# Performance work log

Hardware: AMD Instinct MI355X
Metric: run time of the kernel (lower is better)

## Reference

```python
import jax, jax.numpy as jnp
import numpy as np
import math

EPS = 1e-6
C = 0.01

def _norm(x):
    return jnp.maximum(jnp.linalg.norm(x, axis=-1, keepdims=True), EPS)

def project_to_ball(x, c=C):
    max_norm = 1.0 / math.sqrt(c) - EPS
    norm = _norm(x)
    clamped = jnp.minimum(norm, max_norm - EPS)
    return x * (clamped / norm)

def log_map_zero(x, c=C):
    sqrt_c = math.sqrt(c)
    xn = _norm(x)
    scaled = jnp.minimum(sqrt_c * xn, 1.0 - EPS)
    return jnp.arctanh(scaled) * x / (sqrt_c * xn)

def exp_map_zero(v, c=C):
    sqrt_c = math.sqrt(c)
    vn = _norm(v)
    res = jnp.tanh(sqrt_c * vn) * (v / vn) / sqrt_c
    return project_to_ball(res, c)

def setup_inputs() -> dict:
    key = jax.random.key(0)
    k1, k2, k3 = jax.random.split(key, 3)
    N, d_in, d_out = 262144, 256, 256
    x = jax.random.normal(k1, (N, d_in), dtype=jnp.float32)
    # xavier_uniform with relu gain = sqrt(2)
    gain = math.sqrt(2.0)
    bound = gain * math.sqrt(6.0 / (d_in + d_out))
    W = jax.random.uniform(k2, (d_out, d_in), dtype=jnp.float32, minval=-bound, maxval=bound)
    b = jnp.zeros((d_out,), dtype=jnp.float32)
    return {"x": x, "W": W, "b": b}

def reference(x, W, b):
    tangent = log_map_zero(x)                      # [N, d_in]
    transformed = tangent @ W.T + b                # [N, d_out]
    return exp_map_zero(transformed)               # [N, d_out]
```

## Files before the change

### kernel.cpp

```cpp
#include <hip/hip_runtime.h>
#include <stdint.h>

typedef float f32x4 __attribute__((ext_vector_type(4)));
typedef __bf16 bf16x8 __attribute__((ext_vector_type(8)));

__device__ __forceinline__ unsigned int pack_bf16_rne(float fa, float fb) {
  unsigned int ua = __float_as_uint(fa);
  ua += 0x7fffu + ((ua >> 16) & 1u);
  unsigned int ub = __float_as_uint(fb);
  ub += 0x7fffu + ((ub >> 16) & 1u);
  return __builtin_amdgcn_perm(ub, ua, 0x07060302u);
}

__device__ __forceinline__ void async_cp16(const void* g, void* l) {
  __builtin_amdgcn_global_load_lds(
      (const __attribute__((address_space(1))) unsigned int*)g,
      (__attribute__((address_space(3))) unsigned int*)l, 16, 0, 0);
}

__global__ void wcvt_kernel(const float* __restrict__ W, uint2* __restrict__ Wb) {
  int i = blockIdx.x * blockDim.x + threadIdx.x;
  float4 v = ((const float4*)W)[i];
  uint2 o;
  o.x = pack_bf16_rne(v.x, v.y);
  o.y = pack_bf16_rne(v.z, v.w);
  Wb[i] = o;
}

__global__ __launch_bounds__(256) void hyper_kernel(
    const float* __restrict__ x, const unsigned short* __restrict__ Wb,
    const float* __restrict__ bias, float* __restrict__ out) {
  __shared__ __align__(16) unsigned char As[64 * 256 * 2];
  __shared__ __align__(16) unsigned char Bs[256 * 64 * 2];
  __shared__ float a_scale[64];
  __shared__ float rowsq[64][4];
  __shared__ float oscale[64];

  const int tid = threadIdx.x;
  const int row0 = blockIdx.x * 64;

  {
    const int r = tid >> 2;
    const int j = tid & 3;
    const float4* xr = (const float4*)(x + (size_t)(row0 + r) * 256);
    float ssq = 0.f;
#pragma unroll
    for (int i = 0; i < 8; ++i) {
      int q = j + 4 * i;
      float4 v0 = xr[q * 2];
      float4 v1 = xr[q * 2 + 1];
      ssq += v0.x * v0.x + v0.y * v0.y + v0.z * v0.z + v0.w * v0.w +
             v1.x * v1.x + v1.y * v1.y + v1.z * v1.z + v1.w * v1.w;
      uint4 pk;
      pk.x = pack_bf16_rne(v0.x, v0.y);
      pk.y = pack_bf16_rne(v0.z, v0.w);
      pk.z = pack_bf16_rne(v1.x, v1.y);
      pk.w = pack_bf16_rne(v1.z, v1.w);
      *(uint4*)(As + r * 512 + ((q ^ (r & 7)) << 4)) = pk;
    }
    ssq += __shfl_xor(ssq, 1);
    ssq += __shfl_xor(ssq, 2);
    if (j == 0) {
      float xn = fmaxf(sqrtf(ssq), 1e-6f);
      float t = fminf(0.1f * xn, 1.f - 1e-6f);
      a_scale[r] = atanhf(t) / (0.1f * xn);
    }
  }

  const int wv = tid >> 6;
  const int lane = tid & 63;
  const int l15 = lane & 15;
  const int l4 = lane >> 4;

  const f32x4 fzero = {0.f, 0.f, 0.f, 0.f};
  f32x4 acc[4][4];
#pragma unroll
  for (int a = 0; a < 4; ++a)
#pragma unroll
    for (int b = 0; b < 4; ++b) acc[a][b] = fzero;

  for (int kb = 0; kb < 4; ++kb) {
#pragma unroll
    for (int it = 0; it < 8; ++it) {
      int s = it * 256 + tid;
      int rr = s >> 3, cc = s & 7;
      const unsigned short* g = Wb + rr * 256 + kb * 64 + ((cc ^ (rr & 7)) << 3);
      async_cp16(g, Bs + s * 16);
    }
    __syncthreads();

#pragma unroll
    for (int kk = 0; kk < 2; ++kk) {
      bf16x8 af[4], bfr[4];
#pragma unroll
      for (int t = 0; t < 4; ++t) {
        int ar = t * 16 + l15;
        int qf = kb * 8 + kk * 4 + l4;
        af[t] = *(const bf16x8*)(As + ar * 512 + ((qf ^ (ar & 7)) << 4));
        int br = wv * 64 + t * 16 + l15;
        int qb = kk * 4 + l4;
        bfr[t] = *(const bf16x8*)(Bs + br * 128 + ((qb ^ (br & 7)) << 4));
      }
#pragma unroll
      for (int tr = 0; tr < 4; ++tr)
#pragma unroll
        for (int tc = 0; tc < 4; ++tc)
          acc[tr][tc] = __builtin_amdgcn_mfma_f32_16x16x32_bf16(
              af[tr], bfr[tc], acc[tr][tc], 0, 0, 0);
    }
    __syncthreads();
  }

  float bv[4];
#pragma unroll
  for (int tc = 0; tc < 4; ++tc) bv[tc] = bias[wv * 64 + tc * 16 + l15];

  float p[4][4];
#pragma unroll
  for (int tr = 0; tr < 4; ++tr) {
#pragma unroll
    for (int rg = 0; rg < 4; ++rg) {
      int lr = tr * 16 + l4 * 4 + rg;
      float as = a_scale[lr];
      float s = 0.f;
#pragma unroll
      for (int tc = 0; tc < 4; ++tc) {
        float v = acc[tr][tc][rg] * as + bv[tc];
        acc[tr][tc][rg] = v;
        s += v * v;
      }
      s += __shfl_xor(s, 1);
      s += __shfl_xor(s, 2);
      s += __shfl_xor(s, 4);
      s += __shfl_xor(s, 8);
      p[tr][rg] = s;
    }
  }
  if (l15 == 0) {
#pragma unroll
    for (int tr = 0; tr < 4; ++tr)
#pragma unroll
      for (int rg = 0; rg < 4; ++rg)
        rowsq[tr * 16 + l4 * 4 + rg][wv] = p[tr][rg];
  }
  __syncthreads();
  if (tid < 64) {
    float ssq = rowsq[tid][0] + rowsq[tid][1] + rowsq[tid][2] + rowsq[tid][3];
    float norm = sqrtf(ssq);
    float vn = fmaxf(norm, 1e-6f);
    float a1 = tanhf(0.1f * vn) / (0.1f * vn);
    float rn = fmaxf(norm * a1, 1e-6f);
    float cl = fminf(rn, 10.0f - 2e-6f);
    oscale[tid] = a1 * (cl / rn);
  }
  __syncthreads();

#pragma unroll
  for (int tr = 0; tr < 4; ++tr)
#pragma unroll
    for (int tc = 0; tc < 4; ++tc)
#pragma unroll
      for (int rg = 0; rg < 4; ++rg) {
        int lr = tr * 16 + l4 * 4 + rg;
        out[(size_t)(row0 + lr) * 256 + wv * 64 + tc * 16 + l15] =
            acc[tr][tc][rg] * oscale[lr];
      }
}

extern "C" void kernel_launch(void* const* d_in, const int* in_sizes, int n_in,
                              void* d_out, int out_size, void* d_ws, size_t ws_size,
                              hipStream_t stream) {
  const float* x = (const float*)d_in[0];
  const float* W = (const float*)d_in[1];
  const float* bias = (const float*)d_in[2];
  float* out = (float*)d_out;
  const int N = in_sizes[0] / 256;
  const int wgrid = in_sizes[1] / 1024;

  wcvt_kernel<<<wgrid, 256, 0, stream>>>(W, (uint2*)d_ws);
  hyper_kernel<<<N / 64, 256, 0, stream>>>(x, (const unsigned short*)d_ws, bias, out);
}
```

Before: 461.1 us.

## Persistent kernel with register-resident W and prefetched x tiles

Restructures the fused hyperbolic linear kernel into a persistent grid of 512-thread blocks that loop over 32-row tiles. Each wave keeps its 32-column slice of the bf16 weight matrix in registers for the whole kernel, so W is no longer re-staged through LDS for every tile. The next x tile is loaded into registers while the current tile's MFMA and epilogue run, overlapping global reads with compute. This raises register pressure, and the smaller 32-row tiles carry more per-tile synchronisation overhead.

```diff
diff --git a/kernel.cpp b/kernel.cpp
--- a/kernel.cpp
+++ b/kernel.cpp
@@ -12,12 +12,6 @@
   return __builtin_amdgcn_perm(ub, ua, 0x07060302u);
 }
 
-__device__ __forceinline__ void async_cp16(const void* g, void* l) {
-  __builtin_amdgcn_global_load_lds(
-      (const __attribute__((address_space(1))) unsigned int*)g,
-      (__attribute__((address_space(3))) unsigned int*)l, 16, 0, 0);
-}
-
 __global__ void wcvt_kernel(const float* __restrict__ W, uint2* __restrict__ Wb) {
   int i = blockIdx.x * blockDim.x + threadIdx.x;
   float4 v = ((const float4*)W)[i];
@@ -27,144 +21,159 @@
   Wb[i] = o;
 }
 
-__global__ __launch_bounds__(256) void hyper_kernel(
+__device__ __forceinline__ void convert_tile(float4 g0, float4 g1, float4 g2,
+                                             float4 g3, int lane, int w,
+                                             unsigned char* As, float* a_scale) {
+  float p0 = g0.x * g0.x + g0.y * g0.y + g0.z * g0.z + g0.w * g0.w;
+  float p1 = g1.x * g1.x + g1.y * g1.y + g1.z * g1.z + g1.w * g1.w;
+  float p2 = g2.x * g2.x + g2.y * g2.y + g2.z * g2.z + g2.w * g2.w;
+  float p3 = g3.x * g3.x + g3.y * g3.y + g3.z * g3.z + g3.w * g3.w;
+#pragma unroll
+  for (int m = 1; m < 64; m <<= 1) {
+    p0 += __shfl_xor(p0, m);
+    p1 += __shfl_xor(p1, m);
+    p2 += __shfl_xor(p2, m);
+    p3 += __shfl_xor(p3, m);
+  }
+  float pv = p0;
+  pv = (lane == 1) ? p1 : pv;
+  pv = (lane == 2) ? p2 : pv;
+  pv = (lane == 3) ? p3 : pv;
+  if (lane < 4) {
+    float xn = fmaxf(sqrtf(pv), 1e-6f);
+    float t = fminf(0.1f * xn, 1.0f - 1e-6f);
+    a_scale[w + 8 * lane] = atanhf(t) / (0.1f * xn);
+  }
+  const int physoff = (((lane >> 1) ^ w) << 4) + (lane & 1) * 8;
+#pragma unroll
+  for (int i = 0; i < 4; ++i) {
+    float4 gg = (i == 0) ? g0 : (i == 1) ? g1 : (i == 2) ? g2 : g3;
+    uint2 o;
+    o.x = pack_bf16_rne(gg.x, gg.y);
+    o.y = pack_bf16_rne(gg.z, gg.w);
+    *(uint2*)(As + (w + 8 * i) * 512 + physoff) = o;
+  }
+}
+
+__global__ __launch_bounds__(512, 4) void hyper_kernel(
     const float* __restrict__ x, const unsigned short* __restrict__ Wb,
-    const float* __restrict__ bias, float* __restrict__ out) {
-  __shared__ __align__(16) unsigned char As[64 * 256 * 2];
-  __shared__ __align__(16) unsigned char Bs[256 * 64 * 2];
-  __shared__ float a_scale[64];
-  __shared__ float rowsq[64][4];
-  __shared__ float oscale[64];
+    const float* __restrict__ bias, float* __restrict__ out, int nt) {
+  __shared__ __align__(16) unsigned char As[32 * 512];
+  __shared__ float a_scale[32];
+  __shared__ float rowsq[32][8];
+  __shared__ float oscale[32];
 
   const int tid = threadIdx.x;
-  const int row0 = blockIdx.x * 64;
-
-  {
-    const int r = tid >> 2;
-    const int j = tid & 3;
-    const float4* xr = (const float4*)(x + (size_t)(row0 + r) * 256);
-    float ssq = 0.f;
-#pragma unroll
-    for (int i = 0; i < 8; ++i) {
-      int q = j + 4 * i;
-      float4 v0 = xr[q * 2];
-      float4 v1 = xr[q * 2 + 1];
-      ssq += v0.x * v0.x + v0.y * v0.y + v0.z * v0.z + v0.w * v0.w +
-             v1.x * v1.x + v1.y * v1.y + v1.z * v1.z + v1.w * v1.w;
-      uint4 pk;
-      pk.x = pack_bf16_rne(v0.x, v0.y);
-      pk.y = pack_bf16_rne(v0.z, v0.w);
-      pk.z = pack_bf16_rne(v1.x, v1.y);
-      pk.w = pack_bf16_rne(v1.z, v1.w);
-      *(uint4*)(As + r * 512 + ((q ^ (r & 7)) << 4)) = pk;
-    }
-    ssq += __shfl_xor(ssq, 1);
-    ssq += __shfl_xor(ssq, 2);
-    if (j == 0) {
-      float xn = fmaxf(sqrtf(ssq), 1e-6f);
-      float t = fminf(0.1f * xn, 1.f - 1e-6f);
-      a_scale[r] = atanhf(t) / (0.1f * xn);
-    }
-  }
-
-  const int wv = tid >> 6;
+  const int w = tid >> 6;
   const int lane = tid & 63;
   const int l15 = lane & 15;
   const int l4 = lane >> 4;
+  const int swz = l15 & 7;
 
-  const f32x4 fzero = {0.f, 0.f, 0.f, 0.f};
-  f32x4 acc[4][4];
+  int tile = blockIdx.x;
+  if (tile >= nt) return;
+
+  bf16x8 breg[2][8];
 #pragma unroll
-  for (int a = 0; a < 4; ++a)
+  for (int tc = 0; tc < 2; ++tc) {
+    const unsigned short* wp = Wb + (w * 32 + tc * 16 + l15) * 256 + l4 * 8;
 #pragma unroll
-    for (int b = 0; b < 4; ++b) acc[a][b] = fzero;
+    for (int s = 0; s < 8; ++s) breg[tc][s] = *(const bf16x8*)(wp + s * 32);
+  }
+  float bv[2];
+#pragma unroll
+  for (int tc = 0; tc < 2; ++tc) bv[tc] = bias[w * 32 + tc * 16 + l15];
 
-  for (int kb = 0; kb < 4; ++kb) {
-#pragma unroll
-    for (int it = 0; it < 8; ++it) {
-      int s = it * 256 + tid;
-      int rr = s >> 3, cc = s & 7;
-      const unsigned short* g = Wb + rr * 256 + kb * 64 + ((cc ^ (rr & 7)) << 3);
-      async_cp16(g, Bs + s * 16);
-    }
-    __syncthreads();
-
-#pragma unroll
-    for (int kk = 0; kk < 2; ++kk) {
-      bf16x8 af[4], bfr[4];
-#pragma unroll
-      for (int t = 0; t < 4; ++t) {
-        int ar = t * 16 + l15;
-        int qf = kb * 8 + kk * 4 + l4;
-        af[t] = *(const bf16x8*)(As + ar * 512 + ((qf ^ (ar & 7)) << 4));
-        int br = wv * 64 + t * 16 + l15;
-        int qb = kk * 4 + l4;
-        bfr[t] = *(const bf16x8*)(Bs + br * 128 + ((qb ^ (br & 7)) << 4));
-      }
-#pragma unroll
-      for (int tr = 0; tr < 4; ++tr)
-#pragma unroll
-        for (int tc = 0; tc < 4; ++tc)
-          acc[tr][tc] = __builtin_amdgcn_mfma_f32_16x16x32_bf16(
-              af[tr], bfr[tc], acc[tr][tc], 0, 0, 0);
-    }
-    __syncthreads();
-  }
-
-  float bv[4];
-#pragma unroll
-  for (int tc = 0; tc < 4; ++tc) bv[tc] = bias[wv * 64 + tc * 16 + l15];
-
-  float p[4][4];
-#pragma unroll
-  for (int tr = 0; tr < 4; ++tr) {
-#pragma unroll
-    for (int rg = 0; rg < 4; ++rg) {
-      int lr = tr * 16 + l4 * 4 + rg;
-      float as = a_scale[lr];
-      float s = 0.f;
-#pragma unroll
-      for (int tc = 0; tc < 4; ++tc) {
-        float v = acc[tr][tc][rg] * as + bv[tc];
-        acc[tr][tc][rg] = v;
-        s += v * v;
-      }
-      s += __shfl_xor(s, 1);
-      s += __shfl_xor(s, 2);
-      s += __shfl_xor(s, 4);
-      s += __shfl_xor(s, 8);
-      p[tr][rg] = s;
-    }
-  }
-  if (l15 == 0) {
-#pragma unroll
-    for (int tr = 0; tr < 4; ++tr)
-#pragma unroll
-      for (int rg = 0; rg < 4; ++rg)
-        rowsq[tr * 16 + l4 * 4 + rg][wv] = p[tr][rg];
-  }
-  __syncthreads();
-  if (tid < 64) {
-    float ssq = rowsq[tid][0] + rowsq[tid][1] + rowsq[tid][2] + rowsq[tid][3];
-    float norm = sqrtf(ssq);
-    float vn = fmaxf(norm, 1e-6f);
-    float a1 = tanhf(0.1f * vn) / (0.1f * vn);
-    float rn = fmaxf(norm * a1, 1e-6f);
-    float cl = fminf(rn, 10.0f - 2e-6f);
-    oscale[tid] = a1 * (cl / rn);
+  {
+    const float4* xp = (const float4*)x + (size_t)tile * 2048 + tid;
+    float4 g0 = xp[0], g1 = xp[512], g2 = xp[1024], g3 = xp[1536];
+    convert_tile(g0, g1, g2, g3, lane, w, As, a_scale);
   }
   __syncthreads();
 
+  for (;;) {
+    const int next = tile + (int)gridDim.x;
+    const bool hn = next < nt;
+    float4 g0, g1, g2, g3;
+    if (hn) {
+      const float4* xp = (const float4*)x + (size_t)next * 2048 + tid;
+      g0 = xp[0];
+      g1 = xp[512];
+      g2 = xp[1024];
+      g3 = xp[1536];
+    }
+    __builtin_amdgcn_sched_barrier(0);
+
+    const f32x4 fzero = {0.f, 0.f, 0.f, 0.f};
+    f32x4 acc[2][2];
 #pragma unroll
-  for (int tr = 0; tr < 4; ++tr)
+    for (int a = 0; a < 2; ++a)
 #pragma unroll
-    for (int tc = 0; tc < 4; ++tc)
+      for (int b = 0; b < 2; ++b) acc[a][b] = fzero;
+
+#pragma unroll
+    for (int s = 0; s < 8; ++s) {
+      bf16x8 af[2];
+#pragma unroll
+      for (int tr = 0; tr < 2; ++tr) {
+        int ar = tr * 16 + l15;
+        af[tr] = *(const bf16x8*)(As + ar * 512 + (((s * 4 + l4) ^ swz) << 4));
+      }
+#pragma unroll
+      for (int tr = 0; tr < 2; ++tr)
+#pragma unroll
+        for (int tc = 0; tc < 2; ++tc)
+          acc[tr][tc] = __builtin_amdgcn_mfma_f32_16x16x32_bf16(
+              af[tr], breg[tc][s], acc[tr][tc], 0, 0, 0);
+    }
+
+#pragma unroll
+    for (int tr = 0; tr < 2; ++tr)
 #pragma unroll
       for (int rg = 0; rg < 4; ++rg) {
         int lr = tr * 16 + l4 * 4 + rg;
-        out[(size_t)(row0 + lr) * 256 + wv * 64 + tc * 16 + l15] =
-            acc[tr][tc][rg] * oscale[lr];
+        float as = a_scale[lr];
+        float v0 = acc[tr][0][rg] * as + bv[0];
+        float v1 = acc[tr][1][rg] * as + bv[1];
+        acc[tr][0][rg] = v0;
+        acc[tr][1][rg] = v1;
+        float s = v0 * v0 + v1 * v1;
+        s += __shfl_xor(s, 1);
+        s += __shfl_xor(s, 2);
+        s += __shfl_xor(s, 4);
+        s += __shfl_xor(s, 8);
+        if (l15 == 0) rowsq[lr][w] = s;
       }
+    __syncthreads();
+
+    if (tid < 32) {
+      float ssq = rowsq[tid][0] + rowsq[tid][1] + rowsq[tid][2] + rowsq[tid][3] +
+                  rowsq[tid][4] + rowsq[tid][5] + rowsq[tid][6] + rowsq[tid][7];
+      float norm = sqrtf(ssq);
+      float vn = fmaxf(norm, 1e-6f);
+      float a1 = tanhf(0.1f * vn) / (0.1f * vn);
+      float rn = fmaxf(norm * a1, 1e-6f);
+      float cl = fminf(rn, 10.0f - 2e-6f);
+      oscale[tid] = a1 * (cl / rn);
+    }
+    if (hn) convert_tile(g0, g1, g2, g3, lane, w, As, a_scale);
+    __syncthreads();
+
+    float* op = out + (size_t)tile * 8192 + w * 32 + l15;
+#pragma unroll
+    for (int tr = 0; tr < 2; ++tr)
+#pragma unroll
+      for (int rg = 0; rg < 4; ++rg) {
+        int lr = tr * 16 + l4 * 4 + rg;
+        float os = oscale[lr];
+#pragma unroll
+        for (int tc = 0; tc < 2; ++tc)
+          op[lr * 256 + tc * 16] = acc[tr][tc][rg] * os;
+      }
+
+    if (!hn) break;
+    tile = next;
+  }
 }
 
 extern "C" void kernel_launch(void* const* d_in, const int* in_sizes, int n_in,
@@ -176,7 +185,10 @@
   float* out = (float*)d_out;
   const int N = in_sizes[0] / 256;
   const int wgrid = in_sizes[1] / 1024;
+  const int nt = N / 32;
 
   wcvt_kernel<<<wgrid, 256, 0, stream>>>(W, (uint2*)d_ws);
-  hyper_kernel<<<N / 64, 256, 0, stream>>>(x, (const unsigned short*)d_ws, bias, out);
+  const int grid = nt < 512 ? nt : 512;
+  hyper_kernel<<<grid, 512, 0, stream>>>(x, (const unsigned short*)d_ws, bias,
+                                         out, nt);
 }
```

Result: slower. 472.0 us (+2.4%).
